# Kernel optimization log

Measured on AMD Instinct MI355X. Metric: run time of the kernel, lower is better.

Reference implementation:

```python
import jax, jax.numpy as jnp
import numpy as np

SQ, SK, D, DV = 4096, 4096, 1024, 1024


def setup_inputs() -> dict:
    key = jax.random.key(0)
    kq, kk, kv = jax.random.split(key, 3)
    Q = jax.random.normal(kq, (SQ, D), dtype=jnp.float32)
    K = jax.random.normal(kk, (SK, D), dtype=jnp.float32)
    V = jax.random.normal(kv, (SK, DV), dtype=jnp.float32)
    return {"Q": Q, "K": K, "V": V}


def reference(Q, K, V):
    # scores: [Sq, Sk]; scaled by K.shape[0] (NOT sqrt(d_k)) per original module
    scores = jnp.matmul(Q, K.T) / K.shape[0]
    # softmax over dim=0 (the QUERY axis), matching torch F.softmax(..., dim=0)
    attn = jax.nn.softmax(scores, axis=0)
    return jnp.matmul(attn, V)  # [Sq, Dv]
```

## Files before the change

kernel.cpp:

```cpp
#include <hip/hip_runtime.h>
#include <hip/hip_bf16.h>
#include <stdint.h>

#define SQ_  4096
#define SK_  4096
#define D_   1024
#define DV_  1024

typedef __attribute__((ext_vector_type(4))) float  f32x4;
typedef __attribute__((ext_vector_type(4))) int    i32x4;
typedef __attribute__((ext_vector_type(8))) int    i32x8;

__device__ __forceinline__ unsigned f2fp4(float x) {
  unsigned sgn = (__float_as_uint(x) >> 28) & 0x8u;
  float y = fabsf(x);
  float cs = rintf(y + y);
  float cm = fminf(rintf(y) + 2.0f, 6.0f);
  float c  = (y < 1.75f) ? cs : cm;
  c = (y < 5.0f) ? c : 7.0f;
  return sgn | (unsigned)(int)c;
}

__device__ __forceinline__ void gload_lds16(const void* gp, void* lp) {
  auto g1 = reinterpret_cast<__attribute__((address_space(1))) uint32_t*>(
      reinterpret_cast<uintptr_t>(gp));
  auto l3 = reinterpret_cast<__attribute__((address_space(3))) uint32_t*>(
      reinterpret_cast<uintptr_t>(lp));
  __builtin_amdgcn_global_load_lds(g1, l3, 16, 0, 0);
}

__global__ __launch_bounds__(256, 2)
void prep_kernel(const float* __restrict__ Q, const float* __restrict__ Km,
                 const float* __restrict__ V,
                 unsigned int* __restrict__ Q4, unsigned int* __restrict__ K4,
                 unsigned char* __restrict__ V4t,
                 float* __restrict__ cs_part) {
  __shared__ float tile[64][65];
  __shared__ float csred[4][64];
  int bid = blockIdx.x;
  if (bid < 4096) {
    const int half = SQ_ * D_ / 8;
    int i = bid * 256 + threadIdx.x;
    const float* in = (i < half) ? Q : Km;
    unsigned int* out = (i < half) ? Q4 : K4;
    int ii = (i < half) ? i : i - half;
    const float4* p = reinterpret_cast<const float4*>(in) + (size_t)ii * 2;
    float4 v0 = p[0], v1 = p[1];
    unsigned w = 0;
    w |= f2fp4(2.0f * v0.x);
    w |= f2fp4(2.0f * v0.y) << 4;
    w |= f2fp4(2.0f * v0.z) << 8;
    w |= f2fp4(2.0f * v0.w) << 12;
    w |= f2fp4(2.0f * v1.x) << 16;
    w |= f2fp4(2.0f * v1.y) << 20;
    w |= f2fp4(2.0f * v1.z) << 24;
    w |= f2fp4(2.0f * v1.w) << 28;
    out[ii] = w;
    return;
  }
  int b  = bid - 4096;
  int j0 = (b & 63) * 64;
  int d0 = (b >> 6) * 64;
  int t  = threadIdx.x;
  int tr = t >> 6;
  int tc = t & 63;
  #pragma unroll
  for (int rr = 0; rr < 16; ++rr) {
    int j = rr * 4 + tr;
    tile[j][tc] = V[(size_t)(j0 + j) * DV_ + d0 + tc];
  }
  __syncthreads();
  #pragma unroll
  for (int rr = 0; rr < 16; ++rr) {
    int d = rr * 4 + tr;
    unsigned c = f2fp4(2.0f * tile[tc][d]);
    unsigned pc = __shfl_xor(c, 1, 64);
    if ((tc & 1) == 0)
      V4t[(size_t)(d0 + d) * (SK_ / 2) + (j0 + tc) / 2] =
          (unsigned char)(c | (pc << 4));
  }
  float s = 0.f;
  #pragma unroll
  for (int jj = 0; jj < 16; ++jj) s += tile[tr * 16 + jj][tc];
  csred[tr][tc] = s;
  __syncthreads();
  if (tr == 0)
    cs_part[(size_t)(b & 63) * DV_ + d0 + tc] =
        csred[0][tc] + csred[1][tc] + csred[2][tc] + csred[3][tc];
}

__global__ __launch_bounds__(256, 3)
void gemm1_kernel(const unsigned char* __restrict__ A,
                  const unsigned char* __restrict__ B,
                  unsigned char* __restrict__ E4,
                  int N, float scale) {
  constexpr int KB = D_ / 2;
  constexpr int NT = KB / 64;
  __shared__ __align__(16) unsigned char As[3][128 * 64];
  __shared__ __align__(16) unsigned char Bs[3][128 * 64];

  const int t    = threadIdx.x;
  const int lane = t & 63;
  const int wave = t >> 6;
  const int wr   = wave >> 1, wc = wave & 1;
  const int lr   = lane & 15;
  const int lk   = lane >> 4;

  const int nwg  = gridDim.x * gridDim.y;
  const int orig = blockIdx.y * gridDim.x + blockIdx.x;
  const int cpx  = nwg >> 3;
  const int swz  = (orig & 7) * cpx + (orig >> 3);
  const int bx   = swz % gridDim.x;
  const int by   = swz / gridDim.x;
  const int m0   = by * 128;
  const int n0   = bx * 128;

  auto stage = [&](int buf, int k0B) {
    #pragma unroll
    for (int it = 0; it < 2; ++it) {
      int s = it * 256 + t;
      int row = s >> 2, p = s & 3;
      int pl = p ^ (row & 3);
      gload_lds16(A + (size_t)(m0 + row) * KB + k0B + pl * 16,
                  &As[buf][s * 16]);
    }
    #pragma unroll
    for (int it = 0; it < 2; ++it) {
      int s = it * 256 + t;
      int row = s >> 2, p = s & 3;
      int pl = p ^ (row & 3);
      gload_lds16(B + (size_t)(n0 + row) * KB + k0B + pl * 16,
                  &Bs[buf][s * 16]);
    }
  };

  stage(0, 0);
  stage(1, 64);

  f32x4 acc[4][4] = {};

  int cur = 0;
  #pragma unroll 2
  for (int tt = 0; tt < NT; ++tt) {
    if (tt + 1 < NT) asm volatile("s_waitcnt vmcnt(4)" ::: "memory");
    else             asm volatile("s_waitcnt vmcnt(0)" ::: "memory");
    __builtin_amdgcn_s_barrier();
    asm volatile("" ::: "memory");
    int nb = cur + 2; if (nb >= 3) nb -= 3;
    if (tt + 2 < NT) stage(nb, (tt + 2) * 64);

    i32x4 af[4], bfr[4];
    #pragma unroll
    for (int m = 0; m < 4; ++m) {
      int r = wr * 64 + m * 16 + lr;
      af[m] = *reinterpret_cast<const i32x4*>(
          &As[cur][r * 64 + ((lk ^ (r & 3)) * 16)]);
    }
    #pragma unroll
    for (int n = 0; n < 4; ++n) {
      int r = wc * 64 + n * 16 + lr;
      bfr[n] = *reinterpret_cast<const i32x4*>(
          &Bs[cur][r * 64 + ((lk ^ (r & 3)) * 16)]);
    }

    #pragma unroll
    for (int m = 0; m < 4; ++m)
      #pragma unroll
      for (int n = 0; n < 4; ++n) {
        i32x8 a8, b8;
        a8[0] = af[m][0]; a8[1] = af[m][1];
        a8[2] = af[m][2]; a8[3] = af[m][3];
        a8[4] = 0; a8[5] = 0; a8[6] = 0; a8[7] = 0;
        b8[0] = bfr[n][0]; b8[1] = bfr[n][1];
        b8[2] = bfr[n][2]; b8[3] = bfr[n][3];
        b8[4] = 0; b8[5] = 0; b8[6] = 0; b8[7] = 0;
        acc[m][n] = __builtin_amdgcn_mfma_scale_f32_16x16x128_f8f6f4(
            a8, b8, acc[m][n], 4, 4, 0, 127, 0, 127);
      }
    cur = (cur == 2) ? 0 : cur + 1;
  }

  const int orow0 = m0 + wr * 64 + lk * 4;
  const int ocol0 = n0 + wc * 64 + lr;
  #pragma unroll
  for (int m = 0; m < 4; ++m)
    #pragma unroll
    for (int n = 0; n < 4; ++n)
      #pragma unroll
      for (int r = 0; r < 4; ++r) {
        float s = acc[m][n][r] * scale;
        float e = s + 0.5f * s * s + (1.0f / 6.0f) * s * s * s;
        unsigned c = f2fp4(e * 128.0f);
        unsigned pc = __shfl_xor(c, 1, 64);
        if ((lr & 1) == 0)
          E4[(size_t)(orow0 + m * 16 + r) * (N / 2) +
             ((ocol0 + n * 16) >> 1)] = (unsigned char)(c | (pc << 4));
      }
}

__global__ __launch_bounds__(128, 3)
void gemm2_kernel(const unsigned char* __restrict__ A,
                  const unsigned char* __restrict__ B,
                  float* __restrict__ O,
                  const float* __restrict__ cs_part,
                  int N) {
  constexpr int KB = SK_ / 2;
  constexpr int NT = KB / 64;
  __shared__ __align__(16) unsigned char As[3][64 * 64];
  __shared__ __align__(16) unsigned char Bs[3][128 * 64];
  __shared__ float csL[128];

  const int t    = threadIdx.x;
  const int lane = t & 63;
  const int wave = t >> 6;
  const int lr   = lane & 15;
  const int lk   = lane >> 4;

  const int nwg  = gridDim.x * gridDim.y;
  const int orig = blockIdx.y * gridDim.x + blockIdx.x;
  const int cpx  = nwg >> 3;
  const int swz  = (orig & 7) * cpx + (orig >> 3);
  const int bx   = swz % gridDim.x;
  const int by   = swz / gridDim.x;
  const int m0   = by * 64;
  const int n0   = bx * 128;

  auto stage = [&](int buf, int k0B) {
    #pragma unroll
    for (int it = 0; it < 2; ++it) {
      int s = it * 128 + t;
      int row = s >> 2, p = s & 3;
      int pl = p ^ (row & 3);
      gload_lds16(A + (size_t)(m0 + row) * KB + k0B + pl * 16,
                  &As[buf][s * 16]);
    }
    #pragma unroll
    for (int it = 0; it < 4; ++it) {
      int s = it * 128 + t;
      int row = s >> 2, p = s & 3;
      int pl = p ^ (row & 3);
      gload_lds16(B + (size_t)(n0 + row) * KB + k0B + pl * 16,
                  &Bs[buf][s * 16]);
    }
  };

  stage(0, 0);
  stage(1, 64);

  {
    float s = 0.f;
    #pragma unroll
    for (int p = 0; p < 64; ++p) s += cs_part[(size_t)p * DV_ + n0 + t];
    csL[t] = s;
  }

  f32x4 acc[4][4] = {};

  int cur = 0;
  #pragma unroll 2
  for (int tt = 0; tt < NT; ++tt) {
    if (tt + 1 < NT) asm volatile("s_waitcnt vmcnt(6)" ::: "memory");
    else             asm volatile("s_waitcnt vmcnt(0)" ::: "memory");
    __builtin_amdgcn_s_barrier();
    asm volatile("" ::: "memory");
    int nb = cur + 2; if (nb >= 3) nb -= 3;
    if (tt + 2 < NT) stage(nb, (tt + 2) * 64);

    i32x4 af[4], bfr[4];
    #pragma unroll
    for (int m = 0; m < 4; ++m) {
      int r = m * 16 + lr;
      af[m] = *reinterpret_cast<const i32x4*>(
          &As[cur][r * 64 + ((lk ^ (r & 3)) * 16)]);
    }
    #pragma unroll
    for (int n = 0; n < 4; ++n) {
      int r = wave * 64 + n * 16 + lr;
      bfr[n] = *reinterpret_cast<const i32x4*>(
          &Bs[cur][r * 64 + ((lk ^ (r & 3)) * 16)]);
    }

    #pragma unroll
    for (int m = 0; m < 4; ++m)
      #pragma unroll
      for (int n = 0; n < 4; ++n) {
        i32x8 a8, b8;
        a8[0] = af[m][0]; a8[1] = af[m][1];
        a8[2] = af[m][2]; a8[3] = af[m][3];
        a8[4] = 0; a8[5] = 0; a8[6] = 0; a8[7] = 0;
        b8[0] = bfr[n][0]; b8[1] = bfr[n][1];
        b8[2] = bfr[n][2]; b8[3] = bfr[n][3];
        b8[4] = 0; b8[5] = 0; b8[6] = 0; b8[7] = 0;
        acc[m][n] = __builtin_amdgcn_mfma_scale_f32_16x16x128_f8f6f4(
            a8, b8, acc[m][n], 4, 4, 0, 127, 0, 127);
      }
    cur = (cur == 2) ? 0 : cur + 1;
  }

  const int orow0 = m0 + lk * 4;
  const int ocol0 = n0 + wave * 64 + lr;
  #pragma unroll
  for (int m = 0; m < 4; ++m)
    #pragma unroll
    for (int n = 0; n < 4; ++n) {
      float cs = csL[wave * 64 + n * 16 + lr] * (1.0f / 4096.0f);
      #pragma unroll
      for (int r = 0; r < 4; ++r)
        O[(size_t)(orow0 + m * 16 + r) * N + (ocol0 + n * 16)] =
            cs + acc[m][n][r] * (1.0f / 1048576.0f);
    }
}

extern "C" void kernel_launch(void* const* d_in, const int* in_sizes, int n_in,
                              void* d_out, int out_size, void* d_ws,
                              size_t ws_size, hipStream_t stream) {
  const float* Q = (const float*)d_in[0];
  const float* K = (const float*)d_in[1];
  const float* V = (const float*)d_in[2];

  char* ws = (char*)d_ws;
  unsigned char* Q4   = (unsigned char*)(ws);
  unsigned char* K4   = (unsigned char*)(ws + ((size_t)2 << 20));
  unsigned char* e4   = (unsigned char*)(ws + ((size_t)4 << 20));
  unsigned char* V4t  = (unsigned char*)(ws + ((size_t)12 << 20));
  float*         csp  = (float*)(ws + ((size_t)14 << 20));

  prep_kernel<<<5120, 256, 0, stream>>>(Q, K, V, (unsigned*)Q4, (unsigned*)K4,
                                        V4t, csp);

  gemm1_kernel<<<dim3(SK_ / 128, SQ_ / 128), 256, 0, stream>>>(
      Q4, K4, e4, SK_, 1.0f / 16384.0f);

  gemm2_kernel<<<dim3(DV_ / 128, SQ_ / 64), 128, 0, stream>>>(
      e4, V4t, (float*)d_out, csp, DV_);

  (void)in_sizes; (void)n_in; (void)out_size; (void)ws_size;
}
```

Measured before the change: 59.44 us.

## Move V transpose/quantize into GEMM1 launch, interleaved with GEMM tiles

The V transpose, FP4 quantization and column-sum work moves out of the prep kernel into the first GEMM kernel. Blocks alternate in groups of eight between GEMM tiles and V-transpose tiles, so the memory-bound V work overlaps with the MFMA-bound GEMM. The prep kernel now only converts Q and K. The GEMM blocks use a dynamically carved shared buffer, and the tile swizzle now uses hardcoded grid dimensions. The interleaving may disturb the L2 locality of the GEMM tile order and lengthen the GEMM launch.

```diff
diff --git a/kernel.cpp b/kernel.cpp
--- a/kernel.cpp
+++ b/kernel.cpp
@@ -30,88 +30,90 @@
 }
 
 __global__ __launch_bounds__(256, 2)
-void prep_kernel(const float* __restrict__ Q, const float* __restrict__ Km,
-                 const float* __restrict__ V,
-                 unsigned int* __restrict__ Q4, unsigned int* __restrict__ K4,
-                 unsigned char* __restrict__ V4t,
-                 float* __restrict__ cs_part) {
-  __shared__ float tile[64][65];
-  __shared__ float csred[4][64];
-  int bid = blockIdx.x;
-  if (bid < 4096) {
-    const int half = SQ_ * D_ / 8;
-    int i = bid * 256 + threadIdx.x;
-    const float* in = (i < half) ? Q : Km;
-    unsigned int* out = (i < half) ? Q4 : K4;
-    int ii = (i < half) ? i : i - half;
-    const float4* p = reinterpret_cast<const float4*>(in) + (size_t)ii * 2;
-    float4 v0 = p[0], v1 = p[1];
-    unsigned w = 0;
-    w |= f2fp4(2.0f * v0.x);
-    w |= f2fp4(2.0f * v0.y) << 4;
-    w |= f2fp4(2.0f * v0.z) << 8;
-    w |= f2fp4(2.0f * v0.w) << 12;
-    w |= f2fp4(2.0f * v1.x) << 16;
-    w |= f2fp4(2.0f * v1.y) << 20;
-    w |= f2fp4(2.0f * v1.z) << 24;
-    w |= f2fp4(2.0f * v1.w) << 28;
-    out[ii] = w;
+void conv_kernel(const float* __restrict__ Q, const float* __restrict__ Km,
+                 unsigned int* __restrict__ Q4, unsigned int* __restrict__ K4) {
+  const int half = SQ_ * D_ / 8;
+  int i = blockIdx.x * 256 + threadIdx.x;
+  const float* in = (i < half) ? Q : Km;
+  unsigned int* out = (i < half) ? Q4 : K4;
+  int ii = (i < half) ? i : i - half;
+  const float4* p = reinterpret_cast<const float4*>(in) + (size_t)ii * 2;
+  float4 v0 = p[0], v1 = p[1];
+  unsigned w = 0;
+  w |= f2fp4(2.0f * v0.x);
+  w |= f2fp4(2.0f * v0.y) << 4;
+  w |= f2fp4(2.0f * v0.z) << 8;
+  w |= f2fp4(2.0f * v0.w) << 12;
+  w |= f2fp4(2.0f * v1.x) << 16;
+  w |= f2fp4(2.0f * v1.y) << 20;
+  w |= f2fp4(2.0f * v1.z) << 24;
+  w |= f2fp4(2.0f * v1.w) << 28;
+  out[ii] = w;
+}
+
+__global__ __launch_bounds__(256, 3)
+void g1t_kernel(const unsigned char* __restrict__ A,
+                const unsigned char* __restrict__ B,
+                unsigned char* __restrict__ E4,
+                const float* __restrict__ V,
+                unsigned char* __restrict__ V4t,
+                float* __restrict__ cs_part,
+                int N, float scale) {
+  __shared__ __align__(16) unsigned char smem[49152];
+  const int t = threadIdx.x;
+  const int g = blockIdx.x >> 3;
+  const int l = blockIdx.x & 7;
+
+  if (g & 1) {
+    float* tile  = (float*)smem;
+    float* csred = (float*)(smem + 64 * 65 * 4);
+    int b  = (g >> 1) * 8 + l;
+    int j0 = (b & 63) * 64;
+    int d0 = (b >> 6) * 64;
+    int tr = t >> 6;
+    int tc = t & 63;
+    #pragma unroll
+    for (int rr = 0; rr < 16; ++rr) {
+      int j = rr * 4 + tr;
+      tile[j * 65 + tc] = V[(size_t)(j0 + j) * DV_ + d0 + tc];
+    }
+    __syncthreads();
+    #pragma unroll
+    for (int rr = 0; rr < 16; ++rr) {
+      int d = rr * 4 + tr;
+      unsigned c = f2fp4(2.0f * tile[tc * 65 + d]);
+      unsigned pc = __shfl_xor(c, 1, 64);
+      if ((tc & 1) == 0)
+        V4t[(size_t)(d0 + d) * (SK_ / 2) + (j0 + tc) / 2] =
+            (unsigned char)(c | (pc << 4));
+    }
+    float s = 0.f;
+    #pragma unroll
+    for (int jj = 0; jj < 16; ++jj) s += tile[(tr * 16 + jj) * 65 + tc];
+    csred[tr * 64 + tc] = s;
+    __syncthreads();
+    if (tr == 0)
+      cs_part[(size_t)(b & 63) * DV_ + d0 + tc] =
+          csred[0 * 64 + tc] + csred[1 * 64 + tc] +
+          csred[2 * 64 + tc] + csred[3 * 64 + tc];
     return;
   }
-  int b  = bid - 4096;
-  int j0 = (b & 63) * 64;
-  int d0 = (b >> 6) * 64;
-  int t  = threadIdx.x;
-  int tr = t >> 6;
-  int tc = t & 63;
-  #pragma unroll
-  for (int rr = 0; rr < 16; ++rr) {
-    int j = rr * 4 + tr;
-    tile[j][tc] = V[(size_t)(j0 + j) * DV_ + d0 + tc];
-  }
-  __syncthreads();
-  #pragma unroll
-  for (int rr = 0; rr < 16; ++rr) {
-    int d = rr * 4 + tr;
-    unsigned c = f2fp4(2.0f * tile[tc][d]);
-    unsigned pc = __shfl_xor(c, 1, 64);
-    if ((tc & 1) == 0)
-      V4t[(size_t)(d0 + d) * (SK_ / 2) + (j0 + tc) / 2] =
-          (unsigned char)(c | (pc << 4));
-  }
-  float s = 0.f;
-  #pragma unroll
-  for (int jj = 0; jj < 16; ++jj) s += tile[tr * 16 + jj][tc];
-  csred[tr][tc] = s;
-  __syncthreads();
-  if (tr == 0)
-    cs_part[(size_t)(b & 63) * DV_ + d0 + tc] =
-        csred[0][tc] + csred[1][tc] + csred[2][tc] + csred[3][tc];
-}
-
-__global__ __launch_bounds__(256, 3)
-void gemm1_kernel(const unsigned char* __restrict__ A,
-                  const unsigned char* __restrict__ B,
-                  unsigned char* __restrict__ E4,
-                  int N, float scale) {
+
   constexpr int KB = D_ / 2;
   constexpr int NT = KB / 64;
-  __shared__ __align__(16) unsigned char As[3][128 * 64];
-  __shared__ __align__(16) unsigned char Bs[3][128 * 64];
-
-  const int t    = threadIdx.x;
+  unsigned char* As = smem;
+  unsigned char* Bs = smem + 3 * 128 * 64;
+
   const int lane = t & 63;
   const int wave = t >> 6;
   const int wr   = wave >> 1, wc = wave & 1;
   const int lr   = lane & 15;
   const int lk   = lane >> 4;
 
-  const int nwg  = gridDim.x * gridDim.y;
-  const int orig = blockIdx.y * gridDim.x + blockIdx.x;
-  const int cpx  = nwg >> 3;
-  const int swz  = (orig & 7) * cpx + (orig >> 3);
-  const int bx   = swz % gridDim.x;
-  const int by   = swz / gridDim.x;
+  const int orig = (g >> 1) * 8 + l;
+  const int swz  = (orig & 7) * 128 + (orig >> 3);
+  const int bx   = swz % 32;
+  const int by   = swz / 32;
   const int m0   = by * 128;
   const int n0   = bx * 128;
 
@@ -122,7 +124,7 @@
       int row = s >> 2, p = s & 3;
       int pl = p ^ (row & 3);
       gload_lds16(A + (size_t)(m0 + row) * KB + k0B + pl * 16,
-                  &As[buf][s * 16]);
+                  As + buf * 8192 + s * 16);
     }
     #pragma unroll
     for (int it = 0; it < 2; ++it) {
@@ -130,7 +132,7 @@
       int row = s >> 2, p = s & 3;
       int pl = p ^ (row & 3);
       gload_lds16(B + (size_t)(n0 + row) * KB + k0B + pl * 16,
-                  &Bs[buf][s * 16]);
+                  Bs + buf * 8192 + s * 16);
     }
   };
 
@@ -154,13 +156,13 @@
     for (int m = 0; m < 4; ++m) {
       int r = wr * 64 + m * 16 + lr;
       af[m] = *reinterpret_cast<const i32x4*>(
-          &As[cur][r * 64 + ((lk ^ (r & 3)) * 16)]);
+          As + cur * 8192 + r * 64 + ((lk ^ (r & 3)) * 16));
     }
     #pragma unroll
     for (int n = 0; n < 4; ++n) {
       int r = wc * 64 + n * 16 + lr;
       bfr[n] = *reinterpret_cast<const i32x4*>(
-          &Bs[cur][r * 64 + ((lk ^ (r & 3)) * 16)]);
+          Bs + cur * 8192 + r * 64 + ((lk ^ (r & 3)) * 16));
     }
 
     #pragma unroll
@@ -325,11 +327,10 @@
   unsigned char* V4t  = (unsigned char*)(ws + ((size_t)12 << 20));
   float*         csp  = (float*)(ws + ((size_t)14 << 20));
 
-  prep_kernel<<<5120, 256, 0, stream>>>(Q, K, V, (unsigned*)Q4, (unsigned*)K4,
-                                        V4t, csp);
-
-  gemm1_kernel<<<dim3(SK_ / 128, SQ_ / 128), 256, 0, stream>>>(
-      Q4, K4, e4, SK_, 1.0f / 16384.0f);
+  conv_kernel<<<4096, 256, 0, stream>>>(Q, K, (unsigned*)Q4, (unsigned*)K4);
+
+  g1t_kernel<<<2048, 256, 0, stream>>>(Q4, K4, e4, V, V4t, csp,
+                                       SK_, 1.0f / 16384.0f);
 
   gemm2_kernel<<<dim3(DV_ / 128, SQ_ / 64), 128, 0, stream>>>(
       e4, V4t, (float*)d_out, csp, DV_);
```

New measurement: 68.07 us. 14.5% more time.
